# Kernel optimization log

Hardware: AMD Instinct MI355X
Metric: run time of the kernel (lower is better)

The kernel has to match this reference:

```python
import jax, jax.numpy as jnp
import numpy as np

EPS = 1e-07


def _softsplat(tenIn, tenFlow):
    # tenIn: [N, C, H, W], tenFlow: [N, 2, H, W]
    N, C, H, W = tenIn.shape
    dtype = tenIn.dtype
    gridX = jnp.arange(W, dtype=dtype)[None, None, :]  # [1,1,W]
    gridY = jnp.arange(H, dtype=dtype)[None, :, None]  # [1,H,1]
    fltX = gridX + tenFlow[:, 0]  # [N,H,W]
    fltY = gridY + tenFlow[:, 1]  # [N,H,W]
    finite = jnp.isfinite(fltX) & jnp.isfinite(fltY)
    fltX = jnp.where(finite, fltX, 0.0)
    fltY = jnp.where(finite, fltY, 0.0)
    nwX = jnp.floor(fltX)
    nwY = jnp.floor(fltY)
    b = jnp.arange(N, dtype=jnp.int32)[:, None, None]  # [N,1,1]
    tenIn_flat = jnp.transpose(tenIn, (0, 2, 3, 1)).reshape(-1, C)  # [N*H*W, C]
    out = jnp.zeros((N * H * W, C), dtype=dtype)
    # four bilinear corners: NW, NE, SW, SE
    for dx, dy in ((0, 0), (1, 0), (0, 1), (1, 1)):
        ix = nwX + dx
        iy = nwY + dy
        # bilinear weight, e.g. NW: (nwX+1-fltX)*(nwY+1-fltY)
        w = (1.0 - jnp.abs(fltX - ix)) * (1.0 - jnp.abs(fltY - iy))
        valid = finite & (ix >= 0) & (ix < W) & (iy >= 0) & (iy < H)
        w = jnp.where(valid, w, 0.0)  # zero-weight replaces torch's masked select
        ixi = jnp.clip(ix.astype(jnp.int32), 0, W - 1)
        iyi = jnp.clip(iy.astype(jnp.int32), 0, H - 1)
        idx = (b * (H * W) + iyi * W + ixi).reshape(-1)  # [N*H*W]
        out = out.at[idx].add(tenIn_flat * w.reshape(-1, 1))
    return jnp.transpose(out.reshape(N, H, W, C), (0, 3, 1, 2))


def setup_inputs() -> dict:
    key = jax.random.key(0)
    k1, k2, k3 = jax.random.split(key, 3)
    N, C, H, W = 4, 3, 1080, 1920
    tenIn = jax.random.normal(k1, (N, C, H, W), dtype=jnp.float32)
    tenFlow = jax.random.normal(k2, (N, 2, H, W), dtype=jnp.float32)
    tenMetric = jax.random.normal(k3, (N, 1, H, W), dtype=jnp.float32)
    return {"tenIn": tenIn, "tenFlow": tenFlow, "tenMetric": tenMetric}


def reference(tenIn, tenFlow, tenMetric):
    # mode='soft': concat [tenIn * exp(metric), exp(metric)], splat, normalize
    m = jnp.exp(tenMetric)
    tenCat = jnp.concatenate([tenIn * m, m], axis=1)  # [N, C+1, H, W]
    tenOut = _softsplat(tenCat, tenFlow)
    # mode_sub is None -> addeps normalization
    return tenOut[:, :-1] / (tenOut[:, -1:] + EPS)
```

## Files before the change

kernel.cpp:

```cpp
#include <hip/hip_runtime.h>
#include <math.h>

#define EPS 1e-7f

constexpr int Nn = 4, Hh = 1080, Ww = 1920;
constexpr int HW = Hh * Ww;
constexpr int TOTAL = Nn * HW;

constexpr int TW = 32, TH = 32;
constexpr int TXN = 60, TYN = 34;
constexpr int REACH = 5;
constexpr float NEAR_MAX = 5.0f;
constexpr int WINW = TW + 2 * REACH;
constexpr int WINH = TH + 2 * REACH;
constexpr int WINSZ = WINW * WINH;
constexpr int NCW = TW + 1;
constexpr int NCH = TH + 1;
constexpr int NCELLS = NCW * NCH;
constexpr int NOFF = NCELLS + 1;
constexpr int PADL = 8;
constexpr int NCHUNK = 12;
constexpr int TOTCH = NCHUNK * WINH;
constexpr float INV64K = 1.52587890625e-5f;


__global__ __launch_bounds__(256) void far_scatter(
    const float* __restrict__ tenIn, const float* __restrict__ tenFlow,
    const float* __restrict__ tenMetric,
    unsigned int* __restrict__ farCount, float* __restrict__ farList,
    unsigned int farCap)
{
    int q = blockIdx.x * 256 + threadIdx.x;
    if (q >= TOTAL / 4) return;
    int n  = q / (HW / 4);
    int p  = (q - n * (HW / 4)) * 4;

    const float* __restrict__ f0 = tenFlow + (size_t)(n * 2 + 0) * HW;
    const float* __restrict__ f1 = f0 + HW;
    float4 fx4 = *(const float4*)(f0 + p);
    float4 fy4 = *(const float4*)(f1 + p);

    float mx = fmaxf(fmaxf(fabsf(fx4.x), fabsf(fx4.y)), fmaxf(fabsf(fx4.z), fabsf(fx4.w)));
    float my = fmaxf(fmaxf(fabsf(fy4.x), fabsf(fy4.y)), fmaxf(fabsf(fy4.z), fabsf(fy4.w)));
    if (!(mx > NEAR_MAX || my > NEAR_MAX)) return;

    int y = p / Ww;
    int xbase = p - y * Ww;
    float fxa[4] = {fx4.x, fx4.y, fx4.z, fx4.w};
    float fya[4] = {fy4.x, fy4.y, fy4.z, fy4.w};

#pragma unroll
    for (int k = 0; k < 4; ++k) {
        float fxv = fxa[k], fyv = fya[k];
        if (!(fabsf(fxv) > NEAR_MAX || fabsf(fyv) > NEAR_MAX)) continue;
        float fx = (float)(xbase + k) + fxv;
        float fy = (float)y + fyv;
        if (!isfinite(fx) || !isfinite(fy)) continue;
        if (!(fx > -1.0f && fx < (float)Ww && fy > -1.0f && fy < (float)Hh)) continue;

        int pp = p + k;
        float m  = expf(tenMetric[(size_t)n * HW + pp]);
        float v0 = tenIn[((size_t)n * 3 + 0) * HW + pp] * m;
        float v1 = tenIn[((size_t)n * 3 + 1) * HW + pp] * m;
        float v2 = tenIn[((size_t)n * 3 + 2) * HW + pp] * m;

        unsigned int slot = atomicAdd(farCount, 1u);
        if (slot < farCap) {
            float* ep = farList + (size_t)slot * 8;
            ep[0] = __int_as_float(n);
            ep[1] = fx; ep[2] = fy;
            ep[3] = v0; ep[4] = v1; ep[5] = v2; ep[6] = m;
            ep[7] = 0.0f;
        }
    }
}


__global__ __launch_bounds__(256, 4) void gather_splat(
    const float* __restrict__ tenIn, const float* __restrict__ tenFlow,
    const float* __restrict__ tenMetric,
    const float* __restrict__ farList, const unsigned int* __restrict__ farCount,
    unsigned int farCap, float* __restrict__ out)
{
    __shared__ float4 sVal[WINSZ];
    __shared__ unsigned int sPack[WINSZ];
    __shared__ unsigned int sOff[NOFF];
    __shared__ unsigned int sWsum[8];

    const int tx = blockIdx.x, ty = blockIdx.y, n = blockIdx.z;
    const int tX = tx * TW, tY = ty * TH;
    const int tid = threadIdx.x;

    for (int j = tid; j < NOFF; j += 256) sOff[j] = 0u;
    __syncthreads();

    const float* __restrict__ f0 = tenFlow   + (size_t)(n * 2 + 0) * HW;
    const float* __restrict__ f1 = tenFlow   + (size_t)(n * 2 + 1) * HW;
    const float* __restrict__ mp = tenMetric + (size_t)n * HW;
    const float* __restrict__ i0 = tenIn + (size_t)(n * 3 + 0) * HW;
    const float* __restrict__ i1 = tenIn + (size_t)(n * 3 + 1) * HW;
    const float* __restrict__ i2 = tenIn + (size_t)(n * 3 + 2) * HW;

    unsigned int pk[2][4];
    unsigned int spw[2][4];

#pragma unroll
    for (int cc = 0; cc < 2; ++cc) {
#pragma unroll
        for (int k = 0; k < 4; ++k) { pk[cc][k] = 0xFFFFFFFFu; spw[cc][k] = 0u; }
        int cidx = tid + cc * 256;
        if (cidx >= TOTCH) continue;
        int wy = cidx / NCHUNK;
        int cx = cidx - wy * NCHUNK;
        int sy = tY - REACH + wy;
        int gx = tX - PADL + cx * 4;
        if (sy < 0 || sy >= Hh || gx < 0 || gx > Ww - 4) continue;
        int p = sy * Ww + gx;
        float4 fx4 = *(const float4*)(f0 + p);
        float4 fy4 = *(const float4*)(f1 + p);
        float fxa[4] = {fx4.x, fx4.y, fx4.z, fx4.w};
        float fya[4] = {fy4.x, fy4.y, fy4.z, fy4.w};
#pragma unroll
        for (int k = 0; k < 4; ++k) {
            int x = gx + k;
            if (x < tX - REACH || x >= tX + TW + REACH) continue;
            float fxv = fxa[k], fyv = fya[k];
            if (!(fabsf(fxv) <= NEAR_MAX && fabsf(fyv) <= NEAR_MAX)) continue;
            float fx = (float)x + fxv;
            float fy = (float)sy + fyv;
            float flx = floorf(fx), fly = floorf(fy);
            int lx0 = (int)flx - tX;
            int ly0 = (int)fly - tY;
            if (lx0 < -1 || lx0 >= TW || ly0 < -1 || ly0 >= TH) continue;
            int ci = (ly0 + 1) * NCW + (lx0 + 1);
            unsigned int sic = atomicAdd(&sOff[ci], 1u);
            pk[cc][k] = (sic << 16) | (unsigned int)ci;
            spw[cc][k] = __float2uint_rz((fx - flx) * 65536.0f)
                       | (__float2uint_rz((fy - fly) * 65536.0f) << 16);
        }
    }
    __syncthreads();

    unsigned int c0v = 0, c1v = 0, c2v = 0, c3v = 0, c4v = 0;
    if (tid < 218) {
        int base = tid * 5;
        c0v = sOff[base];     c1v = sOff[base + 1]; c2v = sOff[base + 2];
        c3v = sOff[base + 3]; c4v = sOff[base + 4];
    }
    unsigned int tsum = c0v + c1v + c2v + c3v + c4v;
    unsigned int incl = tsum;
#pragma unroll
    for (int d = 1; d < 64; d <<= 1) {
        unsigned int v = __shfl_up(incl, d);
        if ((tid & 63) >= d) incl += v;
    }
    const int wv = tid >> 6;
    if ((tid & 63) == 63) sWsum[wv] = incl;
    __syncthreads();
    unsigned int woff = 0;
    {
        unsigned int w0 = sWsum[0], w1 = sWsum[1], w2 = sWsum[2];
        if (wv > 0) woff += w0;
        if (wv > 1) woff += w1;
        if (wv > 2) woff += w2;
    }
    unsigned int texcl = woff + incl - tsum;
    if (tid < 218) {
        int base = tid * 5;
        unsigned int o0 = texcl, o1 = o0 + c0v, o2 = o1 + c1v, o3 = o2 + c2v, o4 = o3 + c3v;
        sOff[base] = o0; sOff[base + 1] = o1; sOff[base + 2] = o2;
        sOff[base + 3] = o3; sOff[base + 4] = o4;
    }
    __syncthreads();

#pragma unroll
    for (int cc = 0; cc < 2; ++cc) {
        int cidx = tid + cc * 256;
        if (cidx >= TOTCH) continue;
        unsigned int allv = pk[cc][0] & pk[cc][1] & pk[cc][2] & pk[cc][3];
        if (allv == 0xFFFFFFFFu) continue;
        int wy = cidx / NCHUNK;
        int cx = cidx - wy * NCHUNK;
        int sy = tY - REACH + wy;
        int gx = tX - PADL + cx * 4;
        int p = sy * Ww + gx;
        float4 m4  = *(const float4*)(mp + p);
        float4 a04 = *(const float4*)(i0 + p);
        float4 a14 = *(const float4*)(i1 + p);
        float4 a24 = *(const float4*)(i2 + p);
        float ma[4]  = {m4.x,  m4.y,  m4.z,  m4.w};
        float a0a[4] = {a04.x, a04.y, a04.z, a04.w};
        float a1a[4] = {a14.x, a14.y, a14.z, a14.w};
        float a2a[4] = {a24.x, a24.y, a24.z, a24.w};
#pragma unroll
        for (int k = 0; k < 4; ++k) {
            unsigned int p_ = pk[cc][k];
            if (p_ == 0xFFFFFFFFu) continue;
            unsigned int ci  = p_ & 0xFFFFu;
            unsigned int sic = p_ >> 16;
            unsigned int slot = sOff[ci] + sic;
            float m = expf(ma[k]);
            sPack[slot] = spw[cc][k];
            sVal[slot]  = make_float4(a0a[k] * m, a1a[k] * m, a2a[k] * m, m);
        }
    }
    __syncthreads();

    const int r   = tid >> 3;
    const int g   = tid & 7;
    const int cc0 = g * 4;

    float4 acc0 = make_float4(0.f, 0.f, 0.f, 0.f);
    float4 acc1 = make_float4(0.f, 0.f, 0.f, 0.f);
    float4 acc2 = make_float4(0.f, 0.f, 0.f, 0.f);
    float4 acc3 = make_float4(0.f, 0.f, 0.f, 0.f);

#define SUBR(S0, S1, ROWA, HASL, HASR, ACCL, ACCR)                        \
    for (unsigned int s = (S0); s < (S1); ++s) {                          \
        unsigned int pw = sPack[s];                                       \
        float4 v = sVal[s];                                               \
        float fracx = (float)(pw & 0xFFFFu) * INV64K;                     \
        float wy1q  = (float)(pw >> 16)     * INV64K;                     \
        float ay = (ROWA) ? wy1q : (1.0f - wy1q);                         \
        float wr = ay * fracx;                                            \
        float wl = ay - wr;                                               \
        if (HASL) { ACCL.x += v.x*wl; ACCL.y += v.y*wl;                   \
                    ACCL.z += v.z*wl; ACCL.w += v.w*wl; }                 \
        if (HASR) { ACCR.x += v.x*wr; ACCR.y += v.y*wr;                   \
                    ACCR.z += v.z*wr; ACCR.w += v.w*wr; }                 \
    }

    {
        const int baseA = r * NCW + cc0;
        unsigned int o0 = sOff[baseA],     o1 = sOff[baseA + 1];
        unsigned int o2 = sOff[baseA + 2], o3 = sOff[baseA + 3];
        unsigned int o4 = sOff[baseA + 4], o5 = sOff[baseA + 5];
        SUBR(o0, o1, true, false, true,  acc0, acc0)
        SUBR(o1, o2, true, true,  true,  acc0, acc1)
        SUBR(o2, o3, true, true,  true,  acc1, acc2)
        SUBR(o3, o4, true, true,  true,  acc2, acc3)
        SUBR(o4, o5, true, true,  false, acc3, acc0)
    }
    {
        const int baseB = (r + 1) * NCW + cc0;
        unsigned int o0 = sOff[baseB],     o1 = sOff[baseB + 1];
        unsigned int o2 = sOff[baseB + 2], o3 = sOff[baseB + 3];
        unsigned int o4 = sOff[baseB + 4], o5 = sOff[baseB + 5];
        SUBR(o0, o1, false, false, true,  acc0, acc0)
        SUBR(o1, o2, false, true,  true,  acc0, acc1)
        SUBR(o2, o3, false, true,  true,  acc1, acc2)
        SUBR(o3, o4, false, true,  true,  acc2, acc3)
        SUBR(o4, o5, false, true,  false, acc3, acc0)
    }
#undef SUBR

    const int gy = tY + r;
    if (gy >= Hh) return;
    const int gx = tX + cc0;

    unsigned int fc = *farCount;
    if (fc > farCap) fc = farCap;
    const float gyf = (float)gy;
    const float gxf = (float)gx;
    for (unsigned int e = 0; e < fc; ++e) {
        const float* ep = farList + (size_t)e * 8;
        if (__float_as_int(ep[0]) != n) continue;
        float ffx = ep[1], ffy = ep[2];
        float ay = fmaxf(0.f, 1.f - fabsf(ffy - gyf));
        if (ay > 0.f) {
            float fv0 = ep[3], fv1 = ep[4], fv2 = ep[5], fm = ep[6];
            float d = ffx - gxf;
            float ax0 = fmaxf(0.f, 1.f - fabsf(d));
            float ax1 = fmaxf(0.f, 1.f - fabsf(d - 1.f));
            float ax2 = fmaxf(0.f, 1.f - fabsf(d - 2.f));
            float ax3 = fmaxf(0.f, 1.f - fabsf(d - 3.f));
            float w0 = ay * ax0, w1 = ay * ax1, w2 = ay * ax2, w3 = ay * ax3;
            acc0.x += fv0 * w0; acc0.y += fv1 * w0; acc0.z += fv2 * w0; acc0.w += fm * w0;
            acc1.x += fv0 * w1; acc1.y += fv1 * w1; acc1.z += fv2 * w1; acc1.w += fm * w1;
            acc2.x += fv0 * w2; acc2.y += fv1 * w2; acc2.z += fv2 * w2; acc2.w += fm * w2;
            acc3.x += fv0 * w3; acc3.y += fv1 * w3; acc3.z += fv2 * w3; acc3.w += fm * w3;
        }
    }

    const float inv0 = 1.0f / (acc0.w + EPS);
    const float inv1 = 1.0f / (acc1.w + EPS);
    const float inv2 = 1.0f / (acc2.w + EPS);
    const float inv3 = 1.0f / (acc3.w + EPS);

    const size_t pix = (size_t)gy * Ww + gx;
    float4 o;
    o = make_float4(acc0.x * inv0, acc1.x * inv1, acc2.x * inv2, acc3.x * inv3);
    *(float4*)(out + ((size_t)n * 3 + 0) * HW + pix) = o;
    o = make_float4(acc0.y * inv0, acc1.y * inv1, acc2.y * inv2, acc3.y * inv3);
    *(float4*)(out + ((size_t)n * 3 + 1) * HW + pix) = o;
    o = make_float4(acc0.z * inv0, acc1.z * inv1, acc2.z * inv2, acc3.z * inv3);
    *(float4*)(out + ((size_t)n * 3 + 2) * HW + pix) = o;
}

extern "C" void kernel_launch(void* const* d_in, const int* in_sizes, int n_in,
                              void* d_out, int out_size, void* d_ws, size_t ws_size,
                              hipStream_t stream) {
    const float* tenIn     = (const float*)d_in[0];
    const float* tenFlow   = (const float*)d_in[1];
    const float* tenMetric = (const float*)d_in[2];
    float* out = (float*)d_out;

    unsigned int* farCount = (unsigned int*)d_ws;
    float* farList = (float*)((char*)d_ws + 64);
    unsigned int farCap = (ws_size > 64) ? (unsigned int)((ws_size - 64) / 32) : 0;

    hipMemsetAsync(d_ws, 0, 64, stream);

    far_scatter<<<(TOTAL / 4 + 255) / 256, 256, 0, stream>>>(
        tenIn, tenFlow, tenMetric, farCount, farList, farCap);

    dim3 grid(TXN, TYN, Nn);
    gather_splat<<<grid, 256, 0, stream>>>(
        tenIn, tenFlow, tenMetric, farList, farCount, farCap, out);
}
```

Before: 291.3 us.

## Use column-major cell bins and load splat inputs in first pass

Cell indices now run column-major (x outer, y inner). Each gather thread can then walk one contiguous sOff range per column covering both source rows, with 5 loops instead of 10. The metric and image loads, exp and premultiply move into the first binning pass and are held in registers until the second pass writes them to shared memory. This drops a second global reload and address recompute, but adds about 32 live registers per thread and a per-element row-select branch in the gather loop.

```diff
diff --git a/kernel.cpp b/kernel.cpp
--- a/kernel.cpp
+++ b/kernel.cpp
@@ -14,9 +14,9 @@
 constexpr int WINW = TW + 2 * REACH;
 constexpr int WINH = TH + 2 * REACH;
 constexpr int WINSZ = WINW * WINH;
-constexpr int NCW = TW + 1;
 constexpr int NCH = TH + 1;
-constexpr int NCELLS = NCW * NCH;
+constexpr int NCWc = TW + 1;
+constexpr int NCELLS = NCWc * NCH;
 constexpr int NOFF = NCELLS + 1;
 constexpr int PADL = 8;
 constexpr int NCHUNK = 12;
@@ -103,11 +103,12 @@
 
     unsigned int pk[2][4];
     unsigned int spw[2][4];
+    float rv0[2][4], rv1[2][4], rv2[2][4], rvm[2][4];
 
 #pragma unroll
     for (int cc = 0; cc < 2; ++cc) {
 #pragma unroll
-        for (int k = 0; k < 4; ++k) { pk[cc][k] = 0xFFFFFFFFu; spw[cc][k] = 0u; }
+        for (int k = 0; k < 4; ++k) pk[cc][k] = 0xFFFFFFFFu;
         int cidx = tid + cc * 256;
         if (cidx >= TOTCH) continue;
         int wy = cidx / NCHUNK;
@@ -118,8 +119,16 @@
         int p = sy * Ww + gx;
         float4 fx4 = *(const float4*)(f0 + p);
         float4 fy4 = *(const float4*)(f1 + p);
+        float4 m4  = *(const float4*)(mp + p);
+        float4 a04 = *(const float4*)(i0 + p);
+        float4 a14 = *(const float4*)(i1 + p);
+        float4 a24 = *(const float4*)(i2 + p);
         float fxa[4] = {fx4.x, fx4.y, fx4.z, fx4.w};
         float fya[4] = {fy4.x, fy4.y, fy4.z, fy4.w};
+        float ma[4]  = {m4.x,  m4.y,  m4.z,  m4.w};
+        float a0a[4] = {a04.x, a04.y, a04.z, a04.w};
+        float a1a[4] = {a14.x, a14.y, a14.z, a14.w};
+        float a2a[4] = {a24.x, a24.y, a24.z, a24.w};
 #pragma unroll
         for (int k = 0; k < 4; ++k) {
             int x = gx + k;
@@ -132,11 +141,16 @@
             int lx0 = (int)flx - tX;
             int ly0 = (int)fly - tY;
             if (lx0 < -1 || lx0 >= TW || ly0 < -1 || ly0 >= TH) continue;
-            int ci = (ly0 + 1) * NCW + (lx0 + 1);
+            int ci = (lx0 + 1) * NCH + (ly0 + 1);
             unsigned int sic = atomicAdd(&sOff[ci], 1u);
             pk[cc][k] = (sic << 16) | (unsigned int)ci;
             spw[cc][k] = __float2uint_rz((fx - flx) * 65536.0f)
                        | (__float2uint_rz((fy - fly) * 65536.0f) << 16);
+            float m = expf(ma[k]);
+            rv0[cc][k] = a0a[k] * m;
+            rv1[cc][k] = a1a[k] * m;
+            rv2[cc][k] = a2a[k] * m;
+            rvm[cc][k] = m;
         }
     }
     __syncthreads();
@@ -175,23 +189,6 @@
 
 #pragma unroll
     for (int cc = 0; cc < 2; ++cc) {
-        int cidx = tid + cc * 256;
-        if (cidx >= TOTCH) continue;
-        unsigned int allv = pk[cc][0] & pk[cc][1] & pk[cc][2] & pk[cc][3];
-        if (allv == 0xFFFFFFFFu) continue;
-        int wy = cidx / NCHUNK;
-        int cx = cidx - wy * NCHUNK;
-        int sy = tY - REACH + wy;
-        int gx = tX - PADL + cx * 4;
-        int p = sy * Ww + gx;
-        float4 m4  = *(const float4*)(mp + p);
-        float4 a04 = *(const float4*)(i0 + p);
-        float4 a14 = *(const float4*)(i1 + p);
-        float4 a24 = *(const float4*)(i2 + p);
-        float ma[4]  = {m4.x,  m4.y,  m4.z,  m4.w};
-        float a0a[4] = {a04.x, a04.y, a04.z, a04.w};
-        float a1a[4] = {a14.x, a14.y, a14.z, a14.w};
-        float a2a[4] = {a24.x, a24.y, a24.z, a24.w};
 #pragma unroll
         for (int k = 0; k < 4; ++k) {
             unsigned int p_ = pk[cc][k];
@@ -199,9 +196,8 @@
             unsigned int ci  = p_ & 0xFFFFu;
             unsigned int sic = p_ >> 16;
             unsigned int slot = sOff[ci] + sic;
-            float m = expf(ma[k]);
             sPack[slot] = spw[cc][k];
-            sVal[slot]  = make_float4(a0a[k] * m, a1a[k] * m, a2a[k] * m, m);
+            sVal[slot]  = make_float4(rv0[cc][k], rv1[cc][k], rv2[cc][k], rvm[cc][k]);
         }
     }
     __syncthreads();
@@ -215,44 +211,32 @@
     float4 acc2 = make_float4(0.f, 0.f, 0.f, 0.f);
     float4 acc3 = make_float4(0.f, 0.f, 0.f, 0.f);
 
-#define SUBR(S0, S1, ROWA, HASL, HASR, ACCL, ACCR)                        \
-    for (unsigned int s = (S0); s < (S1); ++s) {                          \
-        unsigned int pw = sPack[s];                                       \
-        float4 v = sVal[s];                                               \
-        float fracx = (float)(pw & 0xFFFFu) * INV64K;                     \
-        float wy1q  = (float)(pw >> 16)     * INV64K;                     \
-        float ay = (ROWA) ? wy1q : (1.0f - wy1q);                         \
-        float wr = ay * fracx;                                            \
-        float wl = ay - wr;                                               \
-        if (HASL) { ACCL.x += v.x*wl; ACCL.y += v.y*wl;                   \
-                    ACCL.z += v.z*wl; ACCL.w += v.w*wl; }                 \
-        if (HASR) { ACCR.x += v.x*wr; ACCR.y += v.y*wr;                   \
-                    ACCR.z += v.z*wr; ACCR.w += v.w*wr; }                 \
-    }
-
-    {
-        const int baseA = r * NCW + cc0;
-        unsigned int o0 = sOff[baseA],     o1 = sOff[baseA + 1];
-        unsigned int o2 = sOff[baseA + 2], o3 = sOff[baseA + 3];
-        unsigned int o4 = sOff[baseA + 4], o5 = sOff[baseA + 5];
-        SUBR(o0, o1, true, false, true,  acc0, acc0)
-        SUBR(o1, o2, true, true,  true,  acc0, acc1)
-        SUBR(o2, o3, true, true,  true,  acc1, acc2)
-        SUBR(o3, o4, true, true,  true,  acc2, acc3)
-        SUBR(o4, o5, true, true,  false, acc3, acc0)
-    }
-    {
-        const int baseB = (r + 1) * NCW + cc0;
-        unsigned int o0 = sOff[baseB],     o1 = sOff[baseB + 1];
-        unsigned int o2 = sOff[baseB + 2], o3 = sOff[baseB + 3];
-        unsigned int o4 = sOff[baseB + 4], o5 = sOff[baseB + 5];
-        SUBR(o0, o1, false, false, true,  acc0, acc0)
-        SUBR(o1, o2, false, true,  true,  acc0, acc1)
-        SUBR(o2, o3, false, true,  true,  acc1, acc2)
-        SUBR(o3, o4, false, true,  true,  acc2, acc3)
-        SUBR(o4, o5, false, true,  false, acc3, acc0)
-    }
-#undef SUBR
+#define COLRANGE(J, HASL, HASR, ACCL, ACCR)                               \
+    {                                                                     \
+        const int cbase = (cc0 + (J)) * NCH + r;                          \
+        unsigned int lo = sOff[cbase], md = sOff[cbase + 1],              \
+                     hi = sOff[cbase + 2];                                \
+        for (unsigned int s = lo; s < hi; ++s) {                          \
+            unsigned int pw = sPack[s];                                   \
+            float4 v = sVal[s];                                           \
+            float fracx = (float)(pw & 0xFFFFu) * INV64K;                 \
+            float wy1q  = (float)(pw >> 16)     * INV64K;                 \
+            float ay = (s < md) ? wy1q : (1.0f - wy1q);                   \
+            float wr = ay * fracx;                                        \
+            float wl = ay - wr;                                           \
+            if (HASL) { ACCL.x += v.x*wl; ACCL.y += v.y*wl;               \
+                        ACCL.z += v.z*wl; ACCL.w += v.w*wl; }             \
+            if (HASR) { ACCR.x += v.x*wr; ACCR.y += v.y*wr;               \
+                        ACCR.z += v.z*wr; ACCR.w += v.w*wr; }             \
+        }                                                                 \
+    }
+
+    COLRANGE(0, false, true,  acc0, acc0)
+    COLRANGE(1, true,  true,  acc0, acc1)
+    COLRANGE(2, true,  true,  acc1, acc2)
+    COLRANGE(3, true,  true,  acc2, acc3)
+    COLRANGE(4, true,  false, acc3, acc0)
+#undef COLRANGE
 
     const int gy = tY + r;
     if (gy >= Hh) return;
```

Result: slower. 299.3 us (+2.7%).
